# Kernel optimization log

Measured on AMD Instinct MI355X. Metric: run time of the kernel, lower is better.

## Reference

```python
import jax, jax.numpy as jnp
import numpy as np

N_NODES = 100000
N_EDGES = 1600000
D_FEAT = 48


def setup_inputs() -> dict:
    key = jax.random.key(0)
    k1, k2, k3, k4 = jax.random.split(key, 4)
    rows = jax.random.randint(k1, (N_EDGES,), 0, N_NODES, dtype=jnp.int32)
    cols = jax.random.randint(k2, (N_EDGES,), 0, N_NODES, dtype=jnp.int32)
    # normalized adjacency values (positive, like D^-1/2 A D^-1/2 entries)
    vals = jax.random.uniform(k3, (N_EDGES,), dtype=jnp.float32)
    embeds = jax.random.normal(k4, (N_NODES, D_FEAT), dtype=jnp.float32)
    return {"rows": rows, "cols": cols, "vals": vals, "embeds": embeds}


def reference(rows, cols, vals, embeds):
    # torch.spmm(adj, embeds) with adj in COO form:
    # out[i] = sum_{e : rows[e]==i} vals[e] * embeds[cols[e]]
    msgs = vals[:, None] * embeds[cols]          # [E, D] gather + scale
    out = jax.ops.segment_sum(msgs, rows, num_segments=embeds.shape[0])  # [N, D]
    return out
```

## Files before the change

kernel.cpp:

```cpp
#include <hip/hip_runtime.h>


#define N_NODES 100000
#define D_FEAT 48

#define BUCKET_BITS 8
#define BUCKET_NODES 256
#define N_BUCKETS ((N_NODES + BUCKET_NODES - 1) / BUCKET_NODES)
#define CAPB 4608

#define CHUNK 8192
#define P1_THREADS 1024
#define VPT (CHUNK / P1_THREADS / 4)

#define P2_THREADS 256
#define NG (P2_THREADS / 12)

#define OVF_CAP 4096

__global__ __launch_bounds__(P1_THREADS) void partition_kernel(
        const int* __restrict__ rows, const int* __restrict__ cols,
        const float* __restrict__ vals, int* __restrict__ gcur,
        uint2* __restrict__ tmp, uint4* __restrict__ ovf, int* __restrict__ novf,
        int n_edges) {
    __shared__ unsigned skey[CHUNK];
    __shared__ float    sval[CHUNK];
    __shared__ unsigned short sbkt[CHUNK];
    __shared__ int counts[N_BUCKETS];
    __shared__ int bstart[N_BUCKETS];
    __shared__ int cursor[N_BUCKETS];
    __shared__ int gpos[N_BUCKETS];
    __shared__ int wsum[16];

    int t = threadIdx.x;
    int lane = t & 63, w = t >> 6;
    int base = blockIdx.x * CHUNK;
    int n = min(CHUNK, n_edges - base);

    for (int i = t; i < N_BUCKETS; i += P1_THREADS) counts[i] = 0;
    __syncthreads();

    int      b[VPT * 4];
    unsigned key[VPT * 4];
    float    v[VPT * 4];
    const int4*   rows4 = reinterpret_cast<const int4*>(rows + base);
    const int4*   cols4 = reinterpret_cast<const int4*>(cols + base);
    const float4* vals4 = reinterpret_cast<const float4*>(vals + base);
    int n4 = n >> 2;
#pragma unroll
    for (int k = 0; k < VPT; ++k) {
        int idx4 = k * P1_THREADS + t;
        bool ok = idx4 < n4;
        int4   r4 = ok ? rows4[idx4] : make_int4(0, 0, 0, 0);
        int4   c4 = ok ? cols4[idx4] : make_int4(0, 0, 0, 0);
        float4 v4 = ok ? vals4[idx4] : make_float4(0.f, 0.f, 0.f, 0.f);
        int rr[4] = {r4.x, r4.y, r4.z, r4.w};
        int cc[4] = {c4.x, c4.y, c4.z, c4.w};
        float vv[4] = {v4.x, v4.y, v4.z, v4.w};
#pragma unroll
        for (int j = 0; j < 4; ++j) {
            int i = k * 4 + j;
            b[i] = -1;
            if (ok) {
                b[i] = rr[j] >> BUCKET_BITS;
                key[i] = ((unsigned)(rr[j] & (BUCKET_NODES - 1)) << 17) | (unsigned)cc[j];
                v[i] = vv[j];
                atomicAdd(&counts[b[i]], 1);
            }
        }
    }
    __syncthreads();

    int x = (t < N_BUCKETS) ? counts[t] : 0;
#pragma unroll
    for (int d = 1; d < 64; d <<= 1) {
        int y = __shfl_up(x, d, 64);
        if (lane >= d) x += y;
    }
    if (lane == 63) wsum[w] = x;
    __syncthreads();
    if (w == 0) {
        int sv = (lane < 16) ? wsum[lane] : 0;
#pragma unroll
        for (int d = 1; d < 16; d <<= 1) {
            int y = __shfl_up(sv, d, 64);
            if (lane >= d) sv += y;
        }
        if (lane < 16) wsum[lane] = sv;
    }
    __syncthreads();
    if (t < N_BUCKETS) {
        int incl = x + ((w > 0) ? wsum[w - 1] : 0);
        int st = incl - counts[t];
        bstart[t] = st;
        cursor[t] = st;
        gpos[t] = (counts[t] > 0) ? atomicAdd(&gcur[t], counts[t]) : 0;
    }
    __syncthreads();

#pragma unroll
    for (int i = 0; i < VPT * 4; ++i) {
        if (b[i] >= 0) {
            int p = atomicAdd(&cursor[b[i]], 1);
            skey[p] = key[i];
            sval[p] = v[i];
            sbkt[p] = (unsigned short)b[i];
        }
    }
    __syncthreads();

    for (int p = t; p < n; p += P1_THREADS) {
        int bk = sbkt[p];
        int pos = gpos[bk] + (p - bstart[bk]);
        if (pos < CAPB) {
            tmp[(size_t)bk * CAPB + pos] = make_uint2(skey[p], __float_as_uint(sval[p]));
        } else {
            int o = atomicAdd(novf, 1);
            if (o < OVF_CAP) {
                unsigned rl = skey[p] >> 17;
                ovf[o] = make_uint4((unsigned)bk * BUCKET_NODES + rl,
                                    skey[p] & 0x1FFFFu, __float_as_uint(sval[p]), 0u);
            }
        }
    }
}

__global__ __launch_bounds__(P2_THREADS) void accum_kernel(
        const int* __restrict__ gcur, const uint2* __restrict__ tmp,
        const float* __restrict__ embeds, float* __restrict__ out) {
    __shared__ uint2 sorted[CAPB];
    __shared__ int cnt[BUCKET_NODES];
    __shared__ int cur[BUCKET_NODES];
    __shared__ int roff[BUCKET_NODES + 1];
    __shared__ int wsum[4];

    int t = threadIdx.x;
    int lane = t & 63, w = t >> 6;
    int bkt = blockIdx.x;
    const uint2* bucket = tmp + (size_t)bkt * CAPB;
    int cntE = min(gcur[bkt], CAPB);

    cnt[t] = 0;
    __syncthreads();

    for (int idx = t; idx < cntE; idx += P2_THREADS)
        atomicAdd(&cnt[bucket[idx].x >> 17], 1);
    __syncthreads();

    int x = cnt[t];
#pragma unroll
    for (int d = 1; d < 64; d <<= 1) {
        int y = __shfl_up(x, d, 64);
        if (lane >= d) x += y;
    }
    if (lane == 63) wsum[w] = x;
    __syncthreads();
    if (t == 0) {
        int a0 = wsum[0], a1 = wsum[1], a2 = wsum[2];
        wsum[0] = 0; wsum[1] = a0; wsum[2] = a0 + a1; wsum[3] = a0 + a1 + a2;
    }
    __syncthreads();
    {
        int incl = x + wsum[w];
        int st = incl - cnt[t];
        roff[t] = st;
        cur[t] = st;
    }
    if (t == 0) roff[BUCKET_NODES] = cntE;
    __syncthreads();

    for (int idx = t; idx < cntE; idx += P2_THREADS) {
        uint2 pk = bucket[idx];
        int p = atomicAdd(&cur[(int)(pk.x >> 17)], 1);
        sorted[p] = make_uint2(pk.x & 0x1FFFFu, pk.y);
    }
    __syncthreads();

    int g = t / 12;
    int q = t - g * 12;
    if (g < NG) {
        for (int rl = g; rl < BUCKET_NODES; rl += NG) {
            int s = roff[rl], epos = roff[rl + 1];
            float4 a0 = make_float4(0.f, 0.f, 0.f, 0.f);
            float4 a1 = a0, a2 = a0, a3 = a0;
            int e = s;
            for (; e + 3 < epos; e += 4) {
                uint2 p0 = sorted[e + 0];
                uint2 p1 = sorted[e + 1];
                uint2 p2 = sorted[e + 2];
                uint2 p3 = sorted[e + 3];
                float4 m0 = *(reinterpret_cast<const float4*>(embeds + p0.x * D_FEAT) + q);
                float4 m1 = *(reinterpret_cast<const float4*>(embeds + p1.x * D_FEAT) + q);
                float4 m2 = *(reinterpret_cast<const float4*>(embeds + p2.x * D_FEAT) + q);
                float4 m3 = *(reinterpret_cast<const float4*>(embeds + p3.x * D_FEAT) + q);
                float v0 = __uint_as_float(p0.y), v1 = __uint_as_float(p1.y);
                float v2 = __uint_as_float(p2.y), v3 = __uint_as_float(p3.y);
                a0.x += v0 * m0.x; a0.y += v0 * m0.y; a0.z += v0 * m0.z; a0.w += v0 * m0.w;
                a1.x += v1 * m1.x; a1.y += v1 * m1.y; a1.z += v1 * m1.z; a1.w += v1 * m1.w;
                a2.x += v2 * m2.x; a2.y += v2 * m2.y; a2.z += v2 * m2.z; a2.w += v2 * m2.w;
                a3.x += v3 * m3.x; a3.y += v3 * m3.y; a3.z += v3 * m3.z; a3.w += v3 * m3.w;
            }
            for (; e < epos; ++e) {
                uint2 p0 = sorted[e];
                float4 m0 = *(reinterpret_cast<const float4*>(embeds + p0.x * D_FEAT) + q);
                float v0 = __uint_as_float(p0.y);
                a0.x += v0 * m0.x; a0.y += v0 * m0.y; a0.z += v0 * m0.z; a0.w += v0 * m0.w;
            }
            int node = bkt * BUCKET_NODES + rl;
            if (node < N_NODES) {
                float4 r;
                r.x = (a0.x + a1.x) + (a2.x + a3.x);
                r.y = (a0.y + a1.y) + (a2.y + a3.y);
                r.z = (a0.z + a1.z) + (a2.z + a3.z);
                r.w = (a0.w + a1.w) + (a2.w + a3.w);
                *(reinterpret_cast<float4*>(out + (size_t)node * D_FEAT) + q) = r;
            }
        }
    }
}

__global__ void fixup_kernel(const int* __restrict__ novf, const uint4* __restrict__ ovf,
                             const float* __restrict__ embeds, float* __restrict__ out) {
    int n = min(*novf, OVF_CAP);
    int total = n * 12;
    for (int i = blockIdx.x * blockDim.x + threadIdx.x; i < total; i += gridDim.x * blockDim.x) {
        int e = i / 12, q = i % 12;
        uint4 en = ovf[e];
        float4 m = *(reinterpret_cast<const float4*>(embeds + (size_t)en.y * D_FEAT) + q);
        float v = __uint_as_float(en.z);
        float* dst = out + (size_t)en.x * D_FEAT + q * 4;
        atomicAdd(dst + 0, v * m.x);
        atomicAdd(dst + 1, v * m.y);
        atomicAdd(dst + 2, v * m.z);
        atomicAdd(dst + 3, v * m.w);
    }
}

extern "C" void kernel_launch(void* const* d_in, const int* in_sizes, int n_in,
                              void* d_out, int out_size, void* d_ws, size_t ws_size,
                              hipStream_t stream) {
    const int*   rows   = (const int*)d_in[0];
    const int*   cols   = (const int*)d_in[1];
    const float* vals   = (const float*)d_in[2];
    const float* embeds = (const float*)d_in[3];
    float*       out    = (float*)d_out;
    int n_edges = in_sizes[0];

    char* ws = (char*)d_ws;
    int*   gcur = (int*)(ws);
    int*   novf = (int*)(ws + 1600);
    uint4* ovf  = (uint4*)(ws + 4096);
    uint2* tmp  = (uint2*)(ws + 4096 + 65536);

    hipMemsetAsync(ws, 0, 1664, stream);

    int p1_blocks = (n_edges + CHUNK - 1) / CHUNK;
    partition_kernel<<<p1_blocks, P1_THREADS, 0, stream>>>(rows, cols, vals, gcur,
                                                           tmp, ovf, novf, n_edges);
    accum_kernel<<<N_BUCKETS, P2_THREADS, 0, stream>>>(gcur, tmp, embeds, out);
    fixup_kernel<<<8, 256, 0, stream>>>(novf, ovf, embeds, out);
}
```

Baseline: 155.5 us.

## Halve bucket size, scatter partition directly to global, cache bucket edges in registers

```diff
diff --git a/kernel.cpp b/kernel.cpp
--- a/kernel.cpp
+++ b/kernel.cpp
@@ -4,16 +4,17 @@
 #define N_NODES 100000
 #define D_FEAT 48
 
-#define BUCKET_BITS 8
-#define BUCKET_NODES 256
+#define BUCKET_BITS 7
+#define BUCKET_NODES 128
 #define N_BUCKETS ((N_NODES + BUCKET_NODES - 1) / BUCKET_NODES)
-#define CAPB 4608
+#define CAPB 2432
 
 #define CHUNK 8192
 #define P1_THREADS 1024
 #define VPT (CHUNK / P1_THREADS / 4)
 
-#define P2_THREADS 256
+#define P2_THREADS 512
+#define EPT2 ((CAPB + P2_THREADS - 1) / P2_THREADS)
 #define NG (P2_THREADS / 12)
 
 #define OVF_CAP 4096
@@ -23,21 +24,16 @@
         const float* __restrict__ vals, int* __restrict__ gcur,
         uint2* __restrict__ tmp, uint4* __restrict__ ovf, int* __restrict__ novf,
         int n_edges) {
-    __shared__ unsigned skey[CHUNK];
-    __shared__ float    sval[CHUNK];
-    __shared__ unsigned short sbkt[CHUNK];
     __shared__ int counts[N_BUCKETS];
-    __shared__ int bstart[N_BUCKETS];
     __shared__ int cursor[N_BUCKETS];
     __shared__ int gpos[N_BUCKETS];
-    __shared__ int wsum[16];
 
     int t = threadIdx.x;
-    int lane = t & 63, w = t >> 6;
     int base = blockIdx.x * CHUNK;
     int n = min(CHUNK, n_edges - base);
-
-    for (int i = t; i < N_BUCKETS; i += P1_THREADS) counts[i] = 0;
+    int n4 = n >> 2;
+
+    for (int i = t; i < N_BUCKETS; i += P1_THREADS) { counts[i] = 0; cursor[i] = 0; }
     __syncthreads();
 
     int      b[VPT * 4];
@@ -46,7 +42,6 @@
     const int4*   rows4 = reinterpret_cast<const int4*>(rows + base);
     const int4*   cols4 = reinterpret_cast<const int4*>(cols + base);
     const float4* vals4 = reinterpret_cast<const float4*>(vals + base);
-    int n4 = n >> 2;
 #pragma unroll
     for (int k = 0; k < VPT; ++k) {
         int idx4 = k * P1_THREADS + t;
@@ -71,55 +66,24 @@
     }
     __syncthreads();
 
-    int x = (t < N_BUCKETS) ? counts[t] : 0;
-#pragma unroll
-    for (int d = 1; d < 64; d <<= 1) {
-        int y = __shfl_up(x, d, 64);
-        if (lane >= d) x += y;
-    }
-    if (lane == 63) wsum[w] = x;
-    __syncthreads();
-    if (w == 0) {
-        int sv = (lane < 16) ? wsum[lane] : 0;
-#pragma unroll
-        for (int d = 1; d < 16; d <<= 1) {
-            int y = __shfl_up(sv, d, 64);
-            if (lane >= d) sv += y;
-        }
-        if (lane < 16) wsum[lane] = sv;
-    }
-    __syncthreads();
-    if (t < N_BUCKETS) {
-        int incl = x + ((w > 0) ? wsum[w - 1] : 0);
-        int st = incl - counts[t];
-        bstart[t] = st;
-        cursor[t] = st;
-        gpos[t] = (counts[t] > 0) ? atomicAdd(&gcur[t], counts[t]) : 0;
-    }
+    for (int i = t; i < N_BUCKETS; i += P1_THREADS)
+        gpos[i] = (counts[i] > 0) ? atomicAdd(&gcur[i], counts[i]) : 0;
     __syncthreads();
 
 #pragma unroll
     for (int i = 0; i < VPT * 4; ++i) {
         if (b[i] >= 0) {
             int p = atomicAdd(&cursor[b[i]], 1);
-            skey[p] = key[i];
-            sval[p] = v[i];
-            sbkt[p] = (unsigned short)b[i];
-        }
-    }
-    __syncthreads();
-
-    for (int p = t; p < n; p += P1_THREADS) {
-        int bk = sbkt[p];
-        int pos = gpos[bk] + (p - bstart[bk]);
-        if (pos < CAPB) {
-            tmp[(size_t)bk * CAPB + pos] = make_uint2(skey[p], __float_as_uint(sval[p]));
-        } else {
-            int o = atomicAdd(novf, 1);
-            if (o < OVF_CAP) {
-                unsigned rl = skey[p] >> 17;
-                ovf[o] = make_uint4((unsigned)bk * BUCKET_NODES + rl,
-                                    skey[p] & 0x1FFFFu, __float_as_uint(sval[p]), 0u);
+            int pos = gpos[b[i]] + p;
+            if (pos < CAPB) {
+                tmp[(size_t)b[i] * CAPB + pos] = make_uint2(key[i], __float_as_uint(v[i]));
+            } else {
+                int o = atomicAdd(novf, 1);
+                if (o < OVF_CAP) {
+                    unsigned rl = key[i] >> 17;
+                    ovf[o] = make_uint4((unsigned)b[i] * BUCKET_NODES + rl,
+                                        key[i] & 0x1FFFFu, __float_as_uint(v[i]), 0u);
+                }
             }
         }
     }
@@ -132,36 +96,49 @@
     __shared__ int cnt[BUCKET_NODES];
     __shared__ int cur[BUCKET_NODES];
     __shared__ int roff[BUCKET_NODES + 1];
-    __shared__ int wsum[4];
+    __shared__ int ws2[2];
 
     int t = threadIdx.x;
-    int lane = t & 63, w = t >> 6;
+    int lane = t & 63;
     int bkt = blockIdx.x;
     const uint2* bucket = tmp + (size_t)bkt * CAPB;
     int cntE = min(gcur[bkt], CAPB);
 
-    cnt[t] = 0;
-    __syncthreads();
-
-    for (int idx = t; idx < cntE; idx += P2_THREADS)
-        atomicAdd(&cnt[bucket[idx].x >> 17], 1);
-    __syncthreads();
-
-    int x = cnt[t];
-#pragma unroll
-    for (int d = 1; d < 64; d <<= 1) {
-        int y = __shfl_up(x, d, 64);
-        if (lane >= d) x += y;
-    }
-    if (lane == 63) wsum[w] = x;
-    __syncthreads();
-    if (t == 0) {
-        int a0 = wsum[0], a1 = wsum[1], a2 = wsum[2];
-        wsum[0] = 0; wsum[1] = a0; wsum[2] = a0 + a1; wsum[3] = a0 + a1 + a2;
-    }
-    __syncthreads();
-    {
-        int incl = x + wsum[w];
+    if (t < BUCKET_NODES) cnt[t] = 0;
+    __syncthreads();
+
+    unsigned kcol[EPT2];
+    unsigned vbits[EPT2];
+    int      erl[EPT2];
+#pragma unroll
+    for (int j = 0; j < EPT2; ++j) {
+        int idx = t + j * P2_THREADS;
+        erl[j] = -1;
+        if (idx < cntE) {
+            uint2 pk = bucket[idx];
+            erl[j] = (int)(pk.x >> 17);
+            kcol[j] = pk.x & 0x1FFFFu;
+            vbits[j] = pk.y;
+            atomicAdd(&cnt[erl[j]], 1);
+        }
+    }
+    __syncthreads();
+
+    int x = 0;
+    if (t < BUCKET_NODES) {
+        x = cnt[t];
+#pragma unroll
+        for (int d = 1; d < 64; d <<= 1) {
+            int y = __shfl_up(x, d, 64);
+            if (lane >= d) x += y;
+        }
+        if (lane == 63) ws2[t >> 6] = x;
+    }
+    __syncthreads();
+    if (t == 0) { int a = ws2[0]; ws2[0] = 0; ws2[1] = a; }
+    __syncthreads();
+    if (t < BUCKET_NODES) {
+        int incl = x + ws2[t >> 6];
         int st = incl - cnt[t];
         roff[t] = st;
         cur[t] = st;
@@ -169,10 +146,12 @@
     if (t == 0) roff[BUCKET_NODES] = cntE;
     __syncthreads();
 
-    for (int idx = t; idx < cntE; idx += P2_THREADS) {
-        uint2 pk = bucket[idx];
-        int p = atomicAdd(&cur[(int)(pk.x >> 17)], 1);
-        sorted[p] = make_uint2(pk.x & 0x1FFFFu, pk.y);
+#pragma unroll
+    for (int j = 0; j < EPT2; ++j) {
+        if (erl[j] >= 0) {
+            int p = atomicAdd(&cur[erl[j]], 1);
+            sorted[p] = make_uint2(kcol[j], vbits[j]);
+        }
     }
     __syncthreads();
 
@@ -248,11 +227,11 @@
 
     char* ws = (char*)d_ws;
     int*   gcur = (int*)(ws);
-    int*   novf = (int*)(ws + 1600);
+    int*   novf = (int*)(ws + 3200);
     uint4* ovf  = (uint4*)(ws + 4096);
     uint2* tmp  = (uint2*)(ws + 4096 + 65536);
 
-    hipMemsetAsync(ws, 0, 1664, stream);
+    hipMemsetAsync(ws, 0, 3264, stream);
 
     int p1_blocks = (n_edges + CHUNK - 1) / CHUNK;
     partition_kernel<<<p1_blocks, P1_THREADS, 0, stream>>>(rows, cols, vals, gcur,
```

After: 153.2 us. Within noise of the previous version (-1.5%).
